# Performance work log

Measured on AMD Instinct MI355X. Metric: run time of the kernel, lower is better.

Reference implementation:

```python
import jax, jax.numpy as jnp
from jax import lax
import numpy as np

EPS = 1e-5


def adder2d(x, w):
    """AdderNet 'conv': out[b,o,h,w] = -sum_{c,kh,kw} |x_patch - w[o,c,kh,kw]|, stride 1, VALID."""
    O, C, K, _ = w.shape
    # patches: [B, C*K*K, H', W'], feature dim ordered (c, kh, kw) matching w.reshape(O, -1)
    patches = lax.conv_general_dilated_patches(x, (K, K), (1, 1), 'VALID')
    wf = w.reshape(O, C * K * K)
    # broadcast: [B, O, CKK, H', W'] -> reduce CKK
    d = jnp.abs(patches[:, None, :, :, :] - wf[None, :, :, None, None])
    return -d.sum(axis=2)


def batchnorm(x, gamma, beta):
    # training-mode BatchNorm2d: batch statistics over (N, H, W), biased variance
    mean = x.mean(axis=(0, 2, 3), keepdims=True)
    var = x.var(axis=(0, 2, 3), keepdims=True)
    inv = lax.rsqrt(var + EPS)
    return gamma[None, :, None, None] * (x - mean) * inv + beta[None, :, None, None]


def maxpool2x2(x):
    return lax.reduce_window(x, -jnp.inf, lax.max, (1, 1, 2, 2), (1, 1, 2, 2), 'VALID')


def setup_inputs() -> dict:
    key = jax.random.key(0)
    ks = jax.random.split(key, 8)
    B = 128
    x = jax.random.normal(ks[0], (B, 1, 28, 28), dtype=jnp.float32)
    w1 = jax.random.normal(ks[1], (20, 1, 5, 5), dtype=jnp.float32) * 0.2
    w2 = jax.random.normal(ks[2], (50, 20, 5, 5), dtype=jnp.float32) * 0.063  # ~1/sqrt(500)
    gamma1 = jnp.ones((20,), jnp.float32)
    beta1 = jnp.zeros((20,), jnp.float32)
    gamma2 = jnp.ones((50,), jnp.float32)
    beta2 = jnp.zeros((50,), jnp.float32)
    fc1_w = jax.random.normal(ks[3], (500, 800), dtype=jnp.float32) * 0.035
    fc1_b = jnp.zeros((500,), jnp.float32)
    fc2_w = jax.random.normal(ks[4], (10, 500), dtype=jnp.float32) * 0.045
    fc2_b = jnp.zeros((10,), jnp.float32)
    return {"x": x, "w1": w1, "gamma1": gamma1, "beta1": beta1,
            "w2": w2, "gamma2": gamma2, "beta2": beta2,
            "fc1_w": fc1_w, "fc1_b": fc1_b, "fc2_w": fc2_w, "fc2_b": fc2_b}


def reference(x, w1, gamma1, beta1, w2, gamma2, beta2, fc1_w, fc1_b, fc2_w, fc2_b):
    h = adder2d(x, w1)                 # [B,20,24,24]
    h = batchnorm(h, gamma1, beta1)
    h = maxpool2x2(h)                  # [B,20,12,12]
    h = adder2d(h, w2)                 # [B,50,8,8]
    h = batchnorm(h, gamma2, beta2)
    h = maxpool2x2(h)                  # [B,50,4,4]
    h = h.reshape(h.shape[0], 800)
    h = jax.nn.relu(h @ fc1_w.T + fc1_b)
    logits = h @ fc2_w.T + fc2_b       # [B,10]
    return jax.nn.softmax(logits, axis=1)
```

## Files before the change

### kernel.cpp

```cpp
#include <hip/hip_runtime.h>
#include <hip/hip_bf16.h>
#include <math.h>


#define B_N 128
#define EPSBN 1e-5f
#define NCOPY 16

__global__ __launch_bounds__(256) void prep_kernel(
    const float* __restrict__ w2, float* __restrict__ w2t,
    float* __restrict__ sums) {
  int idx = blockIdx.x * 256 + threadIdx.x;
  if (idx < 32000) {
    int o = idx & 63, t = idx >> 6, k = t % 25, c = t / 25;
    w2t[idx] = (o < 50) ? w2[o * 500 + c * 25 + k] : 0.f;
  } else {
    int j = idx - 32000;
    if (j < NCOPY * 140) sums[j] = 0.f;
  }
}

__global__ __launch_bounds__(256) void adder1_bn_kernel(
    const float* __restrict__ x, const float* __restrict__ w1,
    float* __restrict__ out, float* __restrict__ sums) {
  __shared__ float csum[40];
  if (threadIdx.x < 40) csum[threadIdx.x] = 0.f;
  __syncthreads();
  int idx = blockIdx.x * 256 + threadIdx.x;
  int owc = idx % 3; int t = idx / 3;
  int oh  = t % 24;  t /= 24;
  int o   = t % 20;  int b = t / 20;
  const float* xb = x + b * 784;
  const float* wb = w1 + o * 25;
  float acc[8];
#pragma unroll
  for (int i = 0; i < 8; ++i) acc[i] = 0.f;
#pragma unroll
  for (int kh = 0; kh < 5; ++kh) {
    float xr[12];
    const float4* xp = (const float4*)(xb + (oh + kh) * 28 + owc * 8);
#pragma unroll
    for (int i = 0; i < 3; ++i) {
      float4 v = xp[i];
      xr[4*i] = v.x; xr[4*i+1] = v.y; xr[4*i+2] = v.z; xr[4*i+3] = v.w;
    }
    float wr[5];
#pragma unroll
    for (int i = 0; i < 5; ++i) wr[i] = wb[kh * 5 + i];
#pragma unroll
    for (int ow = 0; ow < 8; ++ow)
#pragma unroll
      for (int kw = 0; kw < 5; ++kw)
        acc[ow] += fabsf(xr[ow + kw] - wr[kw]);
  }
  float* op = out + (((size_t)b * 20 + o) * 24 + oh) * 24 + owc * 8;
  float4 s0 = { -acc[0], -acc[1], -acc[2], -acc[3] };
  float4 s1 = { -acc[4], -acc[5], -acc[6], -acc[7] };
  *(float4*)(op)     = s0;
  *(float4*)(op + 4) = s1;
  float s = 0.f, s2 = 0.f;
#pragma unroll
  for (int i = 0; i < 8; ++i) { s -= acc[i]; s2 += acc[i] * acc[i]; }
  atomicAdd(&csum[o * 2],     s);
  atomicAdd(&csum[o * 2 + 1], s2);
  __syncthreads();
  if (threadIdx.x < 40) {
    float v = csum[threadIdx.x];
    if (v != 0.f)
      atomicAdd(&sums[(blockIdx.x & (NCOPY - 1)) * 40 + threadIdx.x], v);
  }
}

__global__ __launch_bounds__(256) void adder2_bn_kernel(
    const float* __restrict__ h1, const float* __restrict__ sums1,
    const float* __restrict__ g1, const float* __restrict__ be1,
    const float* __restrict__ w2t,
    float* __restrict__ out, float* __restrict__ sums2) {
  __shared__ float lh[1440];
  __shared__ float sb[40];
  __shared__ float csum[100];
  const int tid = threadIdx.x;
  if (tid < 100) csum[tid] = 0.f;
  if (tid < 20) {
    float sm = 0.f, s2 = 0.f;
#pragma unroll
    for (int cp = 0; cp < NCOPY; ++cp) {
      sm += sums1[cp * 40 + 2 * tid];
      s2 += sums1[cp * 40 + 2 * tid + 1];
    }
    const float inv_n = 1.f / (B_N * 576);
    float mean = sm * inv_n;
    float var  = s2 * inv_n - mean * mean;
    float sc   = g1[tid] * rsqrtf(var + EPSBN);
    sb[2 * tid]     = sc;
    sb[2 * tid + 1] = be1[tid] - mean * sc;
  }
  __syncthreads();

  const int oq = blockIdx.x & 3;
  const int b  = blockIdx.x >> 2;

  {
    const float* hb = h1 + (size_t)b * 11520;
    for (int j = tid; j < 1440; j += 256) {
      int c = j / 72, rem = j - c * 72;
      int r = rem / 12, col = rem - r * 12;
      const float* hp = hb + (c * 24 + (4 * oq + 2 * r)) * 24 + 2 * col;
      float2 r0 = *(const float2*)(hp);
      float2 r1 = *(const float2*)(hp + 24);
      float sc = sb[2 * c], bi = sb[2 * c + 1];
      float v0 = fmaf(sc, r0.x, bi);
      float v1 = fmaf(sc, r0.y, bi);
      float v2 = fmaf(sc, r1.x, bi);
      float v3 = fmaf(sc, r1.y, bi);
      lh[j] = fmaxf(fmaxf(v0, v1), fmaxf(v2, v3));
    }
  }
  __syncthreads();

  const int o   = tid >> 2;
  const int q   = tid & 3;
  const int ohl = q >> 1;
  const int owh = q & 1;
  if (o < 50) {
    float acc[4];
#pragma unroll
    for (int i = 0; i < 4; ++i) acc[i] = 0.f;
    for (int c = 0; c < 20; ++c) {
      const float* lc = lh + c * 72 + owh * 4;
      const float* wc = w2t + c * 1600 + o;
#pragma unroll
      for (int kh = 0; kh < 5; ++kh) {
        float hr[8];
        const float* lp = lc + (ohl + kh) * 12;
        *(float4*)(hr)     = *(const float4*)(lp);
        *(float4*)(hr + 4) = *(const float4*)(lp + 4);
        float wr[5];
#pragma unroll
        for (int i = 0; i < 5; ++i) wr[i] = wc[(kh * 5 + i) * 64];
#pragma unroll
        for (int ow = 0; ow < 4; ++ow)
#pragma unroll
          for (int kw = 0; kw < 5; ++kw)
            acc[ow] += fabsf(hr[ow + kw] - wr[kw]);
      }
    }
    const int oh = 2 * oq + ohl;
    float4 st = { -acc[0], -acc[1], -acc[2], -acc[3] };
    *(float4*)(out + (((size_t)b * 50 + o) * 8 + oh) * 8 + owh * 4) = st;
    float s = 0.f, s2 = 0.f;
#pragma unroll
    for (int i = 0; i < 4; ++i) { s -= acc[i]; s2 += acc[i] * acc[i]; }
    atomicAdd(&csum[o * 2],     s);
    atomicAdd(&csum[o * 2 + 1], s2);
  }
  __syncthreads();
  if (tid < 100)
    atomicAdd(&sums2[(blockIdx.x & (NCOPY - 1)) * 100 + tid], csum[tid]);
}

__global__ __launch_bounds__(256) void bn_pool_t_kernel(
    const float* __restrict__ h, const float* __restrict__ sums,
    const float* __restrict__ gamma, const float* __restrict__ beta,
    float* __restrict__ outT, float inv_n) {
  int idx = blockIdx.x * 256 + threadIdx.x;
  int pw = idx % 4; int t = idx / 4;
  int ph = t % 4;   t /= 4;
  int c  = t % 50;  int b = t / 50;
  float sm = 0.f, s2 = 0.f;
#pragma unroll
  for (int cp = 0; cp < NCOPY; ++cp) {
    sm += sums[cp * 100 + 2 * c];
    s2 += sums[cp * 100 + 2 * c + 1];
  }
  float mean = sm * inv_n;
  float var  = s2 * inv_n - mean * mean;
  float sc   = gamma[c] * rsqrtf(var + EPSBN);
  float bi   = beta[c] - mean * sc;
  const float* hp = h + ((b * 50 + c) * 8 + 2 * ph) * 8 + 2 * pw;
  float2 r0 = *(const float2*)(hp);
  float2 r1 = *(const float2*)(hp + 8);
  float v0 = fmaf(sc, r0.x, bi);
  float v1 = fmaf(sc, r0.y, bi);
  float v2 = fmaf(sc, r1.x, bi);
  float v3 = fmaf(sc, r1.y, bi);
  int k = (c * 16 + ph * 4 + pw);
  outT[k * 128 + b] = fmaxf(fmaxf(v0, v1), fmaxf(v2, v3));
}

__global__ __launch_bounds__(256) void fc1_kernel(
    const float* __restrict__ featT, const float* __restrict__ w1,
    const float* __restrict__ b1, float* __restrict__ hid) {
  const int j = blockIdx.x;
  const int b = threadIdx.x & 127;
  const int khalf = threadIdx.x >> 7;
  const float* wr = w1 + j * 800;
  const float* fb = featT + b;
  float a0 = 0.f, a1 = 0.f, a2 = 0.f, a3 = 0.f;
  int k0 = khalf * 400;
  for (int k = k0; k < k0 + 400; k += 4) {
    float4 w4 = *(const float4*)(wr + k);
    a0 = fmaf(fb[(k    ) * 128], w4.x, a0);
    a1 = fmaf(fb[(k + 1) * 128], w4.y, a1);
    a2 = fmaf(fb[(k + 2) * 128], w4.z, a2);
    a3 = fmaf(fb[(k + 3) * 128], w4.w, a3);
  }
  __shared__ float part[256];
  part[threadIdx.x] = (a0 + a1) + (a2 + a3);
  __syncthreads();
  if (threadIdx.x < 128)
    hid[b * 512 + j] =
        fmaxf(b1[j] + part[threadIdx.x] + part[threadIdx.x + 128], 0.f);
}

__global__ __launch_bounds__(64) void fc2_softmax_kernel(
    const float* __restrict__ hid, const float* __restrict__ w2,
    const float* __restrict__ b2, float* __restrict__ out) {
  const int b = blockIdx.x, lane = threadIdx.x;
  const float* hb = hid + b * 512;
  __shared__ float logit[16];
  float hv[8];
#pragma unroll
  for (int i = 0; i < 8; ++i) {
    int k = lane + 64 * i;
    hv[i] = (k < 500) ? hb[k] : 0.f;
  }
  for (int j = 0; j < 10; ++j) {
    const float* wr = w2 + j * 500;
    float acc = 0.f;
#pragma unroll
    for (int i = 0; i < 8; ++i) {
      int k = lane + 64 * i;
      float w = (k < 500) ? wr[k] : 0.f;
      acc = fmaf(hv[i], w, acc);
    }
#pragma unroll
    for (int off = 32; off > 0; off >>= 1) acc += __shfl_down(acc, off);
    if (lane == 0) logit[j] = acc + b2[j];
  }
  __syncthreads();
  if (lane == 0) {
    float m = logit[0];
    for (int j = 1; j < 10; ++j) m = fmaxf(m, logit[j]);
    float s = 0.f, e[10];
    for (int j = 0; j < 10; ++j) { e[j] = __expf(logit[j] - m); s += e[j]; }
    float inv = 1.f / s;
    for (int j = 0; j < 10; ++j) out[b * 10 + j] = e[j] * inv;
  }
}

extern "C" void kernel_launch(void* const* d_in, const int* in_sizes, int n_in,
                              void* d_out, int out_size, void* d_ws, size_t ws_size,
                              hipStream_t stream) {
  const float* x   = (const float*)d_in[0];
  const float* w1  = (const float*)d_in[1];
  const float* g1  = (const float*)d_in[2];
  const float* be1 = (const float*)d_in[3];
  const float* w2  = (const float*)d_in[4];
  const float* g2  = (const float*)d_in[5];
  const float* be2 = (const float*)d_in[6];
  const float* fw1 = (const float*)d_in[7];
  const float* fb1 = (const float*)d_in[8];
  const float* fw2 = (const float*)d_in[9];
  const float* fb2 = (const float*)d_in[10];
  float* out = (float*)d_out;

  float* ws    = (float*)d_ws;
  float* h1    = ws;
  float* sums1 = ws + 1843200;
  float* sums2 = ws + 1843840;
  float* w2t   = ws + 1845504;
  float* h2    = ws + 1900000;
  float* featT = ws + 2310000;
  float* hid   = ws + 2420000;

  prep_kernel<<<134, 256, 0, stream>>>(w2, w2t, sums1);
  adder1_bn_kernel<<<720, 256, 0, stream>>>(x, w1, h1, sums1);
  adder2_bn_kernel<<<512, 256, 0, stream>>>(h1, sums1, g1, be1, w2t, h2, sums2);
  bn_pool_t_kernel<<<400, 256, 0, stream>>>(h2, sums2, g2, be2, featT,
                                            1.f / (B_N * 64));
  fc1_kernel<<<500, 256, 0, stream>>>(featT, fw1, fb1, hid);
  fc2_softmax_kernel<<<128, 64, 0, stream>>>(hid, fw2, fb2, out);
}
```

Measured before the change: 141.8 us.

## Fuse prep and BN2-pool into neighbors, replace atomics with per-block stat slots

Removes the separate prep and bn_pool_t kernels. The w2 transpose moves into adder1, and the second pooling is done before normalization inside adder2 by keeping both max and min per window, so fc1 can apply the affine BN using the sign of the scale. Per-block BN partial sums go to dedicated slots that consumers reduce, which removes the global atomics and the zero-init pass. This cuts two launches and the h2 round trip to memory. In exchange, every consumer block redundantly re-reduces all the slots (720 or 512 entries), and the sums are taken in a different order.

New measurement: 160.5 us. 13.2% more time.

```diff
diff --git a/kernel.cpp b/kernel.cpp
--- a/kernel.cpp
+++ b/kernel.cpp
@@ -5,28 +5,17 @@
 
 #define B_N 128
 #define EPSBN 1e-5f
-#define NCOPY 16
-
-__global__ __launch_bounds__(256) void prep_kernel(
-    const float* __restrict__ w2, float* __restrict__ w2t,
-    float* __restrict__ sums) {
-  int idx = blockIdx.x * 256 + threadIdx.x;
-  if (idx < 32000) {
-    int o = idx & 63, t = idx >> 6, k = t % 25, c = t / 25;
-    w2t[idx] = (o < 50) ? w2[o * 500 + c * 25 + k] : 0.f;
-  } else {
-    int j = idx - 32000;
-    if (j < NCOPY * 140) sums[j] = 0.f;
-  }
-}
 
 __global__ __launch_bounds__(256) void adder1_bn_kernel(
     const float* __restrict__ x, const float* __restrict__ w1,
-    float* __restrict__ out, float* __restrict__ sums) {
+    const float* __restrict__ w2,
+    float* __restrict__ out, float* __restrict__ slots1,
+    float* __restrict__ w2t) {
   __shared__ float csum[40];
-  if (threadIdx.x < 40) csum[threadIdx.x] = 0.f;
-  __syncthreads();
-  int idx = blockIdx.x * 256 + threadIdx.x;
+  const int tid = threadIdx.x;
+  if (tid < 40) csum[tid] = 0.f;
+  __syncthreads();
+  int idx = blockIdx.x * 256 + tid;
   int owc = idx % 3; int t = idx / 3;
   int oh  = t % 24;  t /= 24;
   int o   = t % 20;  int b = t / 20;
@@ -64,36 +53,49 @@
   atomicAdd(&csum[o * 2],     s);
   atomicAdd(&csum[o * 2 + 1], s2);
   __syncthreads();
-  if (threadIdx.x < 40) {
-    float v = csum[threadIdx.x];
-    if (v != 0.f)
-      atomicAdd(&sums[(blockIdx.x & (NCOPY - 1)) * 40 + threadIdx.x], v);
+  if (tid < 40) slots1[blockIdx.x * 40 + tid] = csum[tid];
+
+  if (blockIdx.x < 125) {
+    int i = blockIdx.x * 256 + tid;
+    int oo = i & 63, tt = i >> 6, k = tt % 25, c = tt / 25;
+    w2t[i] = (oo < 50) ? w2[oo * 500 + c * 25 + k] : 0.f;
   }
 }
 
 __global__ __launch_bounds__(256) void adder2_bn_kernel(
-    const float* __restrict__ h1, const float* __restrict__ sums1,
+    const float* __restrict__ h1, const float* __restrict__ slots1,
     const float* __restrict__ g1, const float* __restrict__ be1,
     const float* __restrict__ w2t,
-    float* __restrict__ out, float* __restrict__ sums2) {
+    float2* __restrict__ featMM,
+    float* __restrict__ slots2) {
   __shared__ float lh[1440];
-  __shared__ float sb[40];
+  __shared__ float sbb[40];
+  __shared__ float red[240];
   __shared__ float csum[100];
   const int tid = threadIdx.x;
   if (tid < 100) csum[tid] = 0.f;
+
+  if (tid < 240) {
+    int e = tid % 40, seg = tid / 40;
+    float r = 0.f;
+    const float* sp = slots1 + (seg * 120) * 40 + e;
+    for (int i = 0; i < 120; ++i) r += sp[i * 40];
+    red[tid] = r;
+  }
+  __syncthreads();
   if (tid < 20) {
     float sm = 0.f, s2 = 0.f;
 #pragma unroll
-    for (int cp = 0; cp < NCOPY; ++cp) {
-      sm += sums1[cp * 40 + 2 * tid];
-      s2 += sums1[cp * 40 + 2 * tid + 1];
+    for (int sgi = 0; sgi < 6; ++sgi) {
+      sm += red[sgi * 40 + 2 * tid];
+      s2 += red[sgi * 40 + 2 * tid + 1];
     }
     const float inv_n = 1.f / (B_N * 576);
     float mean = sm * inv_n;
     float var  = s2 * inv_n - mean * mean;
     float sc   = g1[tid] * rsqrtf(var + EPSBN);
-    sb[2 * tid]     = sc;
-    sb[2 * tid + 1] = be1[tid] - mean * sc;
+    sbb[2 * tid]     = sc;
+    sbb[2 * tid + 1] = be1[tid] - mean * sc;
   }
   __syncthreads();
 
@@ -108,7 +110,7 @@
       const float* hp = hb + (c * 24 + (4 * oq + 2 * r)) * 24 + 2 * col;
       float2 r0 = *(const float2*)(hp);
       float2 r1 = *(const float2*)(hp + 24);
-      float sc = sb[2 * c], bi = sb[2 * c + 1];
+      float sc = sbb[2 * c], bi = sbb[2 * c + 1];
       float v0 = fmaf(sc, r0.x, bi);
       float v1 = fmaf(sc, r0.y, bi);
       float v2 = fmaf(sc, r1.x, bi);
@@ -145,72 +147,85 @@
             acc[ow] += fabsf(hr[ow + kw] - wr[kw]);
       }
     }
-    const int oh = 2 * oq + ohl;
-    float4 st = { -acc[0], -acc[1], -acc[2], -acc[3] };
-    *(float4*)(out + (((size_t)b * 50 + o) * 8 + oh) * 8 + owh * 4) = st;
-    float s = 0.f, s2 = 0.f;
-#pragma unroll
-    for (int i = 0; i < 4; ++i) { s -= acc[i]; s2 += acc[i] * acc[i]; }
+    float v0 = -acc[0], v1 = -acc[1], v2 = -acc[2], v3 = -acc[3];
+    float s  = v0 + v1 + v2 + v3;
+    float s2 = v0*v0 + v1*v1 + v2*v2 + v3*v3;
     atomicAdd(&csum[o * 2],     s);
     atomicAdd(&csum[o * 2 + 1], s2);
-  }
-  __syncthreads();
-  if (tid < 100)
-    atomicAdd(&sums2[(blockIdx.x & (NCOPY - 1)) * 100 + tid], csum[tid]);
-}
-
-__global__ __launch_bounds__(256) void bn_pool_t_kernel(
-    const float* __restrict__ h, const float* __restrict__ sums,
-    const float* __restrict__ gamma, const float* __restrict__ beta,
-    float* __restrict__ outT, float inv_n) {
-  int idx = blockIdx.x * 256 + threadIdx.x;
-  int pw = idx % 4; int t = idx / 4;
-  int ph = t % 4;   t /= 4;
-  int c  = t % 50;  int b = t / 50;
-  float sm = 0.f, s2 = 0.f;
-#pragma unroll
-  for (int cp = 0; cp < NCOPY; ++cp) {
-    sm += sums[cp * 100 + 2 * c];
-    s2 += sums[cp * 100 + 2 * c + 1];
-  }
-  float mean = sm * inv_n;
-  float var  = s2 * inv_n - mean * mean;
-  float sc   = gamma[c] * rsqrtf(var + EPSBN);
-  float bi   = beta[c] - mean * sc;
-  const float* hp = h + ((b * 50 + c) * 8 + 2 * ph) * 8 + 2 * pw;
-  float2 r0 = *(const float2*)(hp);
-  float2 r1 = *(const float2*)(hp + 8);
-  float v0 = fmaf(sc, r0.x, bi);
-  float v1 = fmaf(sc, r0.y, bi);
-  float v2 = fmaf(sc, r1.x, bi);
-  float v3 = fmaf(sc, r1.y, bi);
-  int k = (c * 16 + ph * 4 + pw);
-  outT[k * 128 + b] = fmaxf(fmaxf(v0, v1), fmaxf(v2, v3));
+    float pM0 = fmaxf(v0, v1), pM1 = fmaxf(v2, v3);
+    float pm0 = fminf(v0, v1), pm1 = fminf(v2, v3);
+    float qM0 = fmaxf(pM0, __shfl_xor(pM0, 2));
+    float qM1 = fmaxf(pM1, __shfl_xor(pM1, 2));
+    float qm0 = fminf(pm0, __shfl_xor(pm0, 2));
+    float qm1 = fminf(pm1, __shfl_xor(pm1, 2));
+    if (ohl == 0) {
+      int k0 = o * 16 + oq * 4 + owh * 2;
+      featMM[(size_t)k0 * 128 + b]       = make_float2(qM0, qm0);
+      featMM[(size_t)(k0 + 1) * 128 + b] = make_float2(qM1, qm1);
+    }
+  }
+  __syncthreads();
+  if (tid < 100) slots2[blockIdx.x * 100 + tid] = csum[tid];
 }
 
 __global__ __launch_bounds__(256) void fc1_kernel(
-    const float* __restrict__ featT, const float* __restrict__ w1,
-    const float* __restrict__ b1, float* __restrict__ hid) {
+    const float2* __restrict__ featMM, const float* __restrict__ slots2,
+    const float* __restrict__ g2, const float* __restrict__ be2,
+    const float* __restrict__ w1, const float* __restrict__ b1,
+    float* __restrict__ hid) {
+  __shared__ float sb2[100];
+  __shared__ float red2[200];
+  __shared__ float part[256];
+  const int tid = threadIdx.x;
+  if (tid < 200) {
+    int e = tid % 100, h = tid / 100;
+    float r = 0.f;
+    const float* sp = slots2 + (h * 256) * 100 + e;
+    for (int i = 0; i < 256; ++i) r += sp[i * 100];
+    red2[tid] = r;
+  }
+  __syncthreads();
+  if (tid < 50) {
+    float sm = red2[2 * tid]     + red2[100 + 2 * tid];
+    float s2 = red2[2 * tid + 1] + red2[100 + 2 * tid + 1];
+    const float inv_n = 1.f / (B_N * 64);
+    float mean = sm * inv_n;
+    float var  = s2 * inv_n - mean * mean;
+    float sc   = g2[tid] * rsqrtf(var + EPSBN);
+    sb2[2 * tid]     = sc;
+    sb2[2 * tid + 1] = be2[tid] - mean * sc;
+  }
+  __syncthreads();
+
   const int j = blockIdx.x;
-  const int b = threadIdx.x & 127;
-  const int khalf = threadIdx.x >> 7;
+  const int b = tid & 127;
+  const int khalf = tid >> 7;
   const float* wr = w1 + j * 800;
-  const float* fb = featT + b;
   float a0 = 0.f, a1 = 0.f, a2 = 0.f, a3 = 0.f;
-  int k0 = khalf * 400;
-  for (int k = k0; k < k0 + 400; k += 4) {
-    float4 w4 = *(const float4*)(wr + k);
-    a0 = fmaf(fb[(k    ) * 128], w4.x, a0);
-    a1 = fmaf(fb[(k + 1) * 128], w4.y, a1);
-    a2 = fmaf(fb[(k + 2) * 128], w4.z, a2);
-    a3 = fmaf(fb[(k + 3) * 128], w4.w, a3);
-  }
-  __shared__ float part[256];
-  part[threadIdx.x] = (a0 + a1) + (a2 + a3);
-  __syncthreads();
-  if (threadIdx.x < 128)
-    hid[b * 512 + j] =
-        fmaxf(b1[j] + part[threadIdx.x] + part[threadIdx.x + 128], 0.f);
+  for (int kg = khalf * 25; kg < khalf * 25 + 25; ++kg) {
+    float sc = sb2[2 * kg], bi = sb2[2 * kg + 1];
+    int kbase = kg * 16;
+#pragma unroll
+    for (int r = 0; r < 16; r += 4) {
+      float4 w4 = *(const float4*)(wr + kbase + r);
+      float2 f0 = featMM[(size_t)(kbase + r    ) * 128 + b];
+      float2 f1 = featMM[(size_t)(kbase + r + 1) * 128 + b];
+      float2 f2 = featMM[(size_t)(kbase + r + 2) * 128 + b];
+      float2 f3 = featMM[(size_t)(kbase + r + 3) * 128 + b];
+      float e0 = fmaf(sc, sc > 0.f ? f0.x : f0.y, bi);
+      float e1 = fmaf(sc, sc > 0.f ? f1.x : f1.y, bi);
+      float e2 = fmaf(sc, sc > 0.f ? f2.x : f2.y, bi);
+      float e3 = fmaf(sc, sc > 0.f ? f3.x : f3.y, bi);
+      a0 = fmaf(e0, w4.x, a0);
+      a1 = fmaf(e1, w4.y, a1);
+      a2 = fmaf(e2, w4.z, a2);
+      a3 = fmaf(e3, w4.w, a3);
+    }
+  }
+  part[tid] = (a0 + a1) + (a2 + a3);
+  __syncthreads();
+  if (tid < 128)
+    hid[b * 512 + j] = fmaxf(b1[j] + part[tid] + part[tid + 128], 0.f);
 }
 
 __global__ __launch_bounds__(64) void fc2_softmax_kernel(
@@ -265,20 +280,17 @@
   const float* fb2 = (const float*)d_in[10];
   float* out = (float*)d_out;
 
-  float* ws    = (float*)d_ws;
-  float* h1    = ws;
-  float* sums1 = ws + 1843200;
-  float* sums2 = ws + 1843840;
-  float* w2t   = ws + 1845504;
-  float* h2    = ws + 1900000;
-  float* featT = ws + 2310000;
-  float* hid   = ws + 2420000;
-
-  prep_kernel<<<134, 256, 0, stream>>>(w2, w2t, sums1);
-  adder1_bn_kernel<<<720, 256, 0, stream>>>(x, w1, h1, sums1);
-  adder2_bn_kernel<<<512, 256, 0, stream>>>(h1, sums1, g1, be1, w2t, h2, sums2);
-  bn_pool_t_kernel<<<400, 256, 0, stream>>>(h2, sums2, g2, be2, featT,
-                                            1.f / (B_N * 64));
-  fc1_kernel<<<500, 256, 0, stream>>>(featT, fw1, fb1, hid);
+  float*  ws     = (float*)d_ws;
+  float*  h1     = ws;
+  float*  slots1 = ws + 1843200;
+  float*  slots2 = ws + 1872128;
+  float*  w2t    = ws + 1923584;
+  float2* featMM = (float2*)(ws + 1956000);
+  float*  hid    = ws + 2170000;
+
+  adder1_bn_kernel<<<720, 256, 0, stream>>>(x, w1, w2, h1, slots1, w2t);
+  adder2_bn_kernel<<<512, 256, 0, stream>>>(h1, slots1, g1, be1, w2t,
+                                            featMM, slots2);
+  fc1_kernel<<<500, 256, 0, stream>>>(featMM, slots2, g2, be2, fw1, fb1, hid);
   fc2_softmax_kernel<<<128, 64, 0, stream>>>(hid, fw2, fb2, out);
 }
```
